# Performance work log

Measured on AMD Instinct MI355X. Metric: run time of the kernel, lower is better.

## Reference

```python
import math
import jax, jax.numpy as jnp
import numpy as np

SCALE = 64.0
MARGIN = 0.5
T = 0.2
COS_M = math.cos(MARGIN)
SIN_M = math.sin(MARGIN)
TH = math.cos(math.pi - MARGIN)
MM = math.sin(math.pi - MARGIN) * MARGIN
EPS = 1e-07

B, D, C = 512, 512, 100000


def setup_inputs() -> dict:
    key = jax.random.key(0)
    k1, k2, k3 = jax.random.split(key, 3)
    embedding = jax.random.normal(k1, (B, D), dtype=jnp.float32)
    # xavier_uniform for (num_classes, embed_size)
    limit = math.sqrt(6.0 / (C + D))
    weight = jax.random.uniform(k2, (C, D), dtype=jnp.float32, minval=-limit, maxval=limit)
    ground_truth = jax.random.randint(k3, (B,), 0, C, dtype=jnp.int64)
    return {"embedding": embedding, "weight": weight, "ground_truth": ground_truth}


def reference(embedding, weight, ground_truth):
    gt = ground_truth.astype(jnp.int32)
    e = embedding / jnp.linalg.norm(embedding, axis=1, keepdims=True)
    w = weight / jnp.linalg.norm(weight, axis=1, keepdims=True)
    # (B, C) cosine similarities
    cos_theta = jnp.clip(jnp.einsum('bd,cd->bc', e, w), -1.0 + EPS, 1.0 - EPS)
    pos = jnp.take_along_axis(cos_theta, gt[:, None], axis=1)  # (B, 1)
    sin_theta = jnp.sqrt(jnp.clip(1.0 - pos * pos, EPS, 1.0 - EPS))
    phi = pos * COS_M - sin_theta * SIN_M
    phi = jnp.where(pos > TH, phi, pos - MM)  # easy_margin=False branch
    # hard-example reweighting: fixed=False -> (t+1)*cos + t where cos > phi
    mask = cos_theta > phi  # phi broadcasts (B,1) -> (B,C)
    cos_theta = jnp.where(mask, (T + 1.0) * cos_theta + T, cos_theta)
    # scatter phi into the ground-truth column
    output = cos_theta.at[jnp.arange(B), gt].set(phi[:, 0])
    output = output * SCALE
    # mean cross-entropy
    logp = jax.nn.log_softmax(output, axis=1)
    loss = -jnp.mean(jnp.take_along_axis(logp, gt[:, None], axis=1))
    return loss
```

## Files before the change

### kernel.cpp

```cpp
#include <hip/hip_runtime.h>
#include <hip/hip_bf16.h>
#include <stdint.h>

typedef unsigned short u16;
typedef __attribute__((ext_vector_type(8))) short short8;
typedef __attribute__((ext_vector_type(4))) float floatx4;

#define B_   512
#define D_   512
#define C_   100000

#define SCALE_  64.0f
#define COSM_   0.8775825618903728f
#define SINM_   0.479425538604203f
#define TH_     (-0.8775825618903728f)
#define MM_     0.2397127693021015f
#define EPS_    1e-7f
#define SHIFT_  89.6f

#define BM 256
#define BN 64
#define BK 32

__device__ inline float wave_reduce_sum(float v) {
    v += __shfl_xor(v, 1);
    v += __shfl_xor(v, 2);
    v += __shfl_xor(v, 4);
    v += __shfl_xor(v, 8);
    v += __shfl_xor(v, 16);
    v += __shfl_xor(v, 32);
    return v;
}

__device__ inline u16 f2bf(float x) {
    union { float f; uint32_t u; } v; v.f = x;
    uint32_t r = v.u + 0x7fffu + ((v.u >> 16) & 1u);
    return (u16)(r >> 16);
}

__global__ __launch_bounds__(256) void norm_e_phi_kernel(
    const float* __restrict__ emb, const float* __restrict__ w_raw,
    const int* __restrict__ gt, u16* __restrict__ e_bf16,
    float* __restrict__ phi, float* __restrict__ rowsum) {
    if (threadIdx.x < 4) rowsum[blockIdx.x * 4 + threadIdx.x] = 0.0f;
    int wv = threadIdx.x >> 6;
    int lane = threadIdx.x & 63;
    int b = blockIdx.x * 4 + wv;
    const float4* rp = (const float4*)(emb + (long)b * D_);
    float4 f0 = rp[lane], f1 = rp[lane + 64];
    float sq = f0.x*f0.x + f0.y*f0.y + f0.z*f0.z + f0.w*f0.w
             + f1.x*f1.x + f1.y*f1.y + f1.z*f1.z + f1.w*f1.w;
    sq = wave_reduce_sum(sq);
    float rn = 1.0f / sqrtf(sq);
    f0.x *= rn; f0.y *= rn; f0.z *= rn; f0.w *= rn;
    f1.x *= rn; f1.y *= rn; f1.z *= rn; f1.w *= rn;
    uint2 p0, p1;
    p0.x = (uint32_t)f2bf(f0.x) | ((uint32_t)f2bf(f0.y) << 16);
    p0.y = (uint32_t)f2bf(f0.z) | ((uint32_t)f2bf(f0.w) << 16);
    p1.x = (uint32_t)f2bf(f1.x) | ((uint32_t)f2bf(f1.y) << 16);
    p1.y = (uint32_t)f2bf(f1.z) | ((uint32_t)f2bf(f1.w) << 16);
    uint2* ob = (uint2*)(e_bf16 + (long)b * D_);
    ob[lane] = p0;
    ob[lane + 64] = p1;

    int g = gt[b];
    const float4* wp = (const float4*)(w_raw + (long)g * D_);
    float4 w0 = wp[lane], w1 = wp[lane + 64];
    float dt = f0.x*w0.x + f0.y*w0.y + f0.z*w0.z + f0.w*w0.w
             + f1.x*w1.x + f1.y*w1.y + f1.z*w1.z + f1.w*w1.w;
    float wsq = w0.x*w0.x + w0.y*w0.y + w0.z*w0.z + w0.w*w0.w
              + w1.x*w1.x + w1.y*w1.y + w1.z*w1.z + w1.w*w1.w;
    dt = wave_reduce_sum(dt);
    wsq = wave_reduce_sum(wsq);
    if (lane == 0) {
        float pos = dt / sqrtf(wsq);
        pos = fminf(fmaxf(pos, -1.0f + EPS_), 1.0f - EPS_);
        float s2 = 1.0f - pos * pos;
        s2 = fminf(fmaxf(s2, EPS_), 1.0f - EPS_);
        float sin_t = sqrtf(s2);
        float ph = pos * COSM_ - sin_t * SINM_;
        ph = (pos > TH_) ? ph : (pos - MM_);
        phi[b] = ph;
    }
}

__device__ inline void cvt_store(const float4& v0, const float4& v1,
                                 u16* dst, float& sq) {
    union { u16 h[8]; uint4 q; } u;
    u.h[0] = f2bf(v0.x); u.h[1] = f2bf(v0.y);
    u.h[2] = f2bf(v0.z); u.h[3] = f2bf(v0.w);
    u.h[4] = f2bf(v1.x); u.h[5] = f2bf(v1.y);
    u.h[6] = f2bf(v1.z); u.h[7] = f2bf(v1.w);
    *(uint4*)dst = u.q;
    sq += v0.x*v0.x + v0.y*v0.y + v0.z*v0.z + v0.w*v0.w
        + v1.x*v1.x + v1.y*v1.y + v1.z*v1.z + v1.w*v1.w;
}

__global__ __launch_bounds__(256, 3) void gemm_arcface_fused(
    const u16* __restrict__ a_g,
    const float* __restrict__ w_g,
    const float* __restrict__ phi, const int* __restrict__ gt,
    float* __restrict__ rowsum) {
    __shared__ __align__(16) u16 b_tile[2][BN * BK];
    __shared__ float phi_s[BM];
    __shared__ int gt_s[BM];
    __shared__ float rnorm_s[BN];

    int tid = threadIdx.x;
    int c0 = (blockIdx.x >> 1) * BN;
    int m0 = (blockIdx.x & 1) * BM;

    phi_s[tid] = phi[m0 + tid];
    gt_s[tid] = gt[m0 + tid];

    int rb = tid >> 2;
    int bslot = tid & 3;
    int bkq = bslot ^ ((rb >> 1) & 3);
    long brow_g = min(c0 + rb, C_ - 1);
    const float4* b_src = (const float4*)(w_g + brow_g * (long)D_ + bkq * 8);
    u16* b_dst0 = &b_tile[0][rb * BK + bslot * 8];
    u16* b_dst1 = &b_tile[1][rb * BK + bslot * 8];

    int wv = tid >> 6, lane = tid & 63;
    int low4 = lane & 15, quad = lane >> 4;
    int lslot = quad ^ ((low4 >> 1) & 3);
    const u16* a_base = a_g + (long)(m0 + wv * 64 + low4) * D_ + quad * 8;
    int bf_off = low4 * BK + lslot * 8;

    floatx4 acc[4][4] = {};
    float sq = 0.0f;
    float4 bv[2][2];
    short8 afc[4];

    bv[0][0] = b_src[0]; bv[0][1] = b_src[1];
    cvt_store(bv[0][0], bv[0][1], b_dst0, sq);
    bv[1][0] = b_src[8]; bv[1][1] = b_src[9];
    __syncthreads();

#pragma unroll
    for (int kt = 0; kt < 16; kt++) {
        int p = kt & 1;
        if (kt < 14) {
            bv[p][0] = b_src[(kt + 2) * 8];
            bv[p][1] = b_src[(kt + 2) * 8 + 1];
        }
#pragma unroll
        for (int mi = 0; mi < 4; mi++)
            afc[mi] = *(const short8*)(a_base + (long)mi * 16 * D_ + kt * BK);
        short8 bf[4];
#pragma unroll
        for (int ni = 0; ni < 4; ni++)
            bf[ni] = *(const short8*)(&b_tile[p][ni * 16 * BK + bf_off]);
#pragma unroll
        for (int mi = 0; mi < 4; mi++)
#pragma unroll
            for (int ni = 0; ni < 4; ni++)
                acc[mi][ni] = __builtin_amdgcn_mfma_f32_16x16x32_bf16(
                    afc[mi], bf[ni], acc[mi][ni], 0, 0, 0);
        if (kt < 15)
            cvt_store(bv[1 - p][0], bv[1 - p][1], p ? b_dst0 : b_dst1, sq);
        __syncthreads();
    }

    sq += __shfl_xor(sq, 1);
    sq += __shfl_xor(sq, 2);
    if ((tid & 3) == 0) rnorm_s[rb] = 1.0f / sqrtf(sq);
    __syncthreads();

#pragma unroll
    for (int mi = 0; mi < 4; mi++) {
#pragma unroll
        for (int r = 0; r < 4; r++) {
            int rl = wv * 64 + mi * 16 + quad * 4 + r;
            float ph = phi_s[rl];
            int g = gt_s[rl];
            float s = 0.0f;
#pragma unroll
            for (int ni = 0; ni < 4; ni++) {
                int cl = ni * 16 + low4;
                int c = c0 + cl;
                float v = acc[mi][ni][r] * rnorm_s[cl];
                v = fminf(fmaxf(v, -1.0f + EPS_), 1.0f - EPS_);
                float logit = (v > ph) ? (1.2f * v + 0.2f) : v;
                logit *= SCALE_;
                if (c == g) logit = SCALE_ * ph;
                s += (c < C_) ? __expf(logit - SHIFT_) : 0.0f;
            }
            s += __shfl_xor(s, 1);
            s += __shfl_xor(s, 2);
            s += __shfl_xor(s, 4);
            s += __shfl_xor(s, 8);
            if (low4 == 0) atomicAdd(&rowsum[m0 + rl], s);
        }
    }
}

__global__ __launch_bounds__(256) void loss_kernel(
    const float* __restrict__ rowsum, const float* __restrict__ phi,
    float* __restrict__ out) {
    __shared__ float red[4];
    int tid = threadIdx.x;
    float s = 0.0f;
    for (int b = tid; b < B_; b += 256)
        s += logf(rowsum[b]) + SHIFT_ - SCALE_ * phi[b];
    s = wave_reduce_sum(s);
    int wv = tid >> 6, lane = tid & 63;
    if (lane == 0) red[wv] = s;
    __syncthreads();
    if (tid == 0) out[0] = (red[0] + red[1] + red[2] + red[3]) * (1.0f / B_);
}

extern "C" void kernel_launch(void* const* d_in, const int* in_sizes, int n_in,
                              void* d_out, int out_size, void* d_ws, size_t ws_size,
                              hipStream_t stream) {
    const float* emb = (const float*)d_in[0];
    const float* wgt = (const float*)d_in[1];
    const int* gt = (const int*)d_in[2];
    float* out = (float*)d_out;

    char* ws = (char*)d_ws;
    u16* e_bf16 = (u16*)(ws);
    float* phi = (float*)(ws + 524288);
    float* rowsum = (float*)(ws + 526336);

    norm_e_phi_kernel<<<B_ / 4, 256, 0, stream>>>(emb, wgt, gt, e_bf16, phi, rowsum);
    int nc = (C_ + BN - 1) / BN;
    gemm_arcface_fused<<<nc * 2, 256, 0, stream>>>(e_bf16, wgt, phi, gt, rowsum);
    loss_kernel<<<1, 256, 0, stream>>>(rowsum, phi, out);
}
```

Measured before the change: 449.0 us.

## Load weight fragments directly from global into registers, dropping LDS staging

The GEMM kernel no longer stages the fp32 weight tile through double-buffered shared memory with per-iteration barriers. Each of the four waves now loads its B fragments straight from global memory, converts them with the packed bf16 intrinsic, and accumulates per-column squared norms that are reduced with cross-lane shuffles. This removes the LDS round trip and 16 barriers, and the occupancy hint rises from 3 to 4 blocks. The cost is that every wave in a block now reads the same 64 weight rows, four times the global/L2 traffic for W, with no software prefetch to hide the load latency.

```diff
diff --git a/kernel.cpp b/kernel.cpp
--- a/kernel.cpp
+++ b/kernel.cpp
@@ -20,7 +20,6 @@
 
 #define BM 256
 #define BN 64
-#define BK 32
 
 __device__ inline float wave_reduce_sum(float v) {
     v += __shfl_xor(v, 1);
@@ -36,6 +35,12 @@
     union { float f; uint32_t u; } v; v.f = x;
     uint32_t r = v.u + 0x7fffu + ((v.u >> 16) & 1u);
     return (u16)(r >> 16);
+}
+
+__device__ inline uint32_t cvt2_rn(float a, float b) {
+    union { __hip_bfloat162 h; uint32_t u; } v;
+    v.h = __float22bfloat162_rn(make_float2(a, b));
+    return v.u;
 }
 
 __global__ __launch_bounds__(256) void norm_e_phi_kernel(
@@ -84,27 +89,13 @@
     }
 }
 
-__device__ inline void cvt_store(const float4& v0, const float4& v1,
-                                 u16* dst, float& sq) {
-    union { u16 h[8]; uint4 q; } u;
-    u.h[0] = f2bf(v0.x); u.h[1] = f2bf(v0.y);
-    u.h[2] = f2bf(v0.z); u.h[3] = f2bf(v0.w);
-    u.h[4] = f2bf(v1.x); u.h[5] = f2bf(v1.y);
-    u.h[6] = f2bf(v1.z); u.h[7] = f2bf(v1.w);
-    *(uint4*)dst = u.q;
-    sq += v0.x*v0.x + v0.y*v0.y + v0.z*v0.z + v0.w*v0.w
-        + v1.x*v1.x + v1.y*v1.y + v1.z*v1.z + v1.w*v1.w;
-}
-
-__global__ __launch_bounds__(256, 3) void gemm_arcface_fused(
+__global__ __launch_bounds__(256, 4) void gemm_arcface_fused(
     const u16* __restrict__ a_g,
     const float* __restrict__ w_g,
     const float* __restrict__ phi, const int* __restrict__ gt,
     float* __restrict__ rowsum) {
-    __shared__ __align__(16) u16 b_tile[2][BN * BK];
     __shared__ float phi_s[BM];
     __shared__ int gt_s[BM];
-    __shared__ float rnorm_s[BN];
 
     int tid = threadIdx.x;
     int c0 = (blockIdx.x >> 1) * BN;
@@ -112,60 +103,58 @@
 
     phi_s[tid] = phi[m0 + tid];
     gt_s[tid] = gt[m0 + tid];
-
-    int rb = tid >> 2;
-    int bslot = tid & 3;
-    int bkq = bslot ^ ((rb >> 1) & 3);
-    long brow_g = min(c0 + rb, C_ - 1);
-    const float4* b_src = (const float4*)(w_g + brow_g * (long)D_ + bkq * 8);
-    u16* b_dst0 = &b_tile[0][rb * BK + bslot * 8];
-    u16* b_dst1 = &b_tile[1][rb * BK + bslot * 8];
+    __syncthreads();
 
     int wv = tid >> 6, lane = tid & 63;
     int low4 = lane & 15, quad = lane >> 4;
-    int lslot = quad ^ ((low4 >> 1) & 3);
+
     const u16* a_base = a_g + (long)(m0 + wv * 64 + low4) * D_ + quad * 8;
-    int bf_off = low4 * BK + lslot * 8;
+    const float4* bp[4];
+#pragma unroll
+    for (int ni = 0; ni < 4; ni++) {
+        int row = min(c0 + ni * 16 + low4, C_ - 1);
+        bp[ni] = (const float4*)(w_g + (long)row * D_ + quad * 8);
+    }
 
     floatx4 acc[4][4] = {};
-    float sq = 0.0f;
-    float4 bv[2][2];
-    short8 afc[4];
-
-    bv[0][0] = b_src[0]; bv[0][1] = b_src[1];
-    cvt_store(bv[0][0], bv[0][1], b_dst0, sq);
-    bv[1][0] = b_src[8]; bv[1][1] = b_src[9];
-    __syncthreads();
+    float sq[4] = {0.0f, 0.0f, 0.0f, 0.0f};
 
 #pragma unroll
     for (int kt = 0; kt < 16; kt++) {
-        int p = kt & 1;
-        if (kt < 14) {
-            bv[p][0] = b_src[(kt + 2) * 8];
-            bv[p][1] = b_src[(kt + 2) * 8 + 1];
+        short8 af[4];
+#pragma unroll
+        for (int mi = 0; mi < 4; mi++)
+            af[mi] = *(const short8*)(a_base + (long)mi * 16 * D_ + kt * 32);
+        short8 bfr[4];
+#pragma unroll
+        for (int ni = 0; ni < 4; ni++) {
+            float4 lo = bp[ni][kt * 8];
+            float4 hi = bp[ni][kt * 8 + 1];
+            sq[ni] += lo.x*lo.x + lo.y*lo.y + lo.z*lo.z + lo.w*lo.w
+                    + hi.x*hi.x + hi.y*hi.y + hi.z*hi.z + hi.w*hi.w;
+            union { short8 s; uint32_t u[4]; } bb;
+            bb.u[0] = cvt2_rn(lo.x, lo.y);
+            bb.u[1] = cvt2_rn(lo.z, lo.w);
+            bb.u[2] = cvt2_rn(hi.x, hi.y);
+            bb.u[3] = cvt2_rn(hi.z, hi.w);
+            bfr[ni] = bb.s;
         }
-#pragma unroll
-        for (int mi = 0; mi < 4; mi++)
-            afc[mi] = *(const short8*)(a_base + (long)mi * 16 * D_ + kt * BK);
-        short8 bf[4];
-#pragma unroll
-        for (int ni = 0; ni < 4; ni++)
-            bf[ni] = *(const short8*)(&b_tile[p][ni * 16 * BK + bf_off]);
 #pragma unroll
         for (int mi = 0; mi < 4; mi++)
 #pragma unroll
             for (int ni = 0; ni < 4; ni++)
                 acc[mi][ni] = __builtin_amdgcn_mfma_f32_16x16x32_bf16(
-                    afc[mi], bf[ni], acc[mi][ni], 0, 0, 0);
-        if (kt < 15)
-            cvt_store(bv[1 - p][0], bv[1 - p][1], p ? b_dst0 : b_dst1, sq);
-        __syncthreads();
-    }
-
-    sq += __shfl_xor(sq, 1);
-    sq += __shfl_xor(sq, 2);
-    if ((tid & 3) == 0) rnorm_s[rb] = 1.0f / sqrtf(sq);
-    __syncthreads();
+                    af[mi], bfr[ni], acc[mi][ni], 0, 0, 0);
+    }
+
+    float rnorm[4];
+#pragma unroll
+    for (int ni = 0; ni < 4; ni++) {
+        float s = sq[ni];
+        s += __shfl_xor(s, 16);
+        s += __shfl_xor(s, 32);
+        rnorm[ni] = 1.0f / sqrtf(s);
+    }
 
 #pragma unroll
     for (int mi = 0; mi < 4; mi++) {
@@ -179,7 +168,7 @@
             for (int ni = 0; ni < 4; ni++) {
                 int cl = ni * 16 + low4;
                 int c = c0 + cl;
-                float v = acc[mi][ni][r] * rnorm_s[cl];
+                float v = acc[mi][ni][r] * rnorm[ni];
                 v = fminf(fmaxf(v, -1.0f + EPS_), 1.0f - EPS_);
                 float logit = (v > ph) ? (1.2f * v + 0.2f) : v;
                 logit *= SCALE_;
```

Result: slower. 1.251 ms (+178.7%).
